# Kernel optimization log

Measured on AMD Instinct MI355X. Metric: run time of the kernel, lower is better.

The kernel has to match this reference:

```python
import jax, jax.numpy as jnp
import numpy as np

NUM_ATOMS = 65536
NUM_BONDS = 131072          # directed bonds; row NUM_BONDS is the zero sentinel h(-1)
MAX_NBR = 4
ATOM_FDIM = 133
CONCAT_FDIM = 147           # atom_fdim + bond_fdim
D_HIDDEN = 300
DEPTH = 3
GF_DIM = 2048
N_MOLS = 4096               # uniform molecules: 16 atoms each


def setup_inputs() -> dict:
    key = jax.random.key(0)
    ks = jax.random.split(key, 9)
    atom_features = jax.random.normal(ks[0], (NUM_ATOMS, ATOM_FDIM), dtype=jnp.float32)
    f_ini_atoms_bonds = jax.random.normal(ks[1], (NUM_BONDS + 1, CONCAT_FDIM), dtype=jnp.float32)
    f_ini_atoms_bonds = f_ini_atoms_bonds.at[-1].set(0.0)  # h(-1) sentinel row
    # indices in [-1, NUM_BONDS-1]; -1 means 'no incoming bond' -> sentinel
    mapping = jax.random.randint(ks[2], (NUM_BONDS + 1, MAX_NBR), -1, NUM_BONDS)
    mapping = mapping.at[-1].set(-1)
    atom_to_incoming_bonds = jax.random.randint(ks[3], (NUM_ATOMS, MAX_NBR), -1, NUM_BONDS)
    global_features = jax.random.normal(ks[4], (N_MOLS, GF_DIM), dtype=jnp.float32)
    W_i = jax.random.normal(ks[5], (D_HIDDEN, CONCAT_FDIM), dtype=jnp.float32) / np.sqrt(CONCAT_FDIM)
    W_h = jax.random.normal(ks[6], (D_HIDDEN, D_HIDDEN), dtype=jnp.float32) / np.sqrt(D_HIDDEN)
    W_o = jax.random.normal(ks[7], (D_HIDDEN, ATOM_FDIM + D_HIDDEN), dtype=jnp.float32) / np.sqrt(ATOM_FDIM + D_HIDDEN)
    b_o = jax.random.normal(ks[8], (D_HIDDEN,), dtype=jnp.float32) * 0.01
    return {
        'atom_features': atom_features,
        'f_ini_atoms_bonds': f_ini_atoms_bonds,
        'atom_to_incoming_bonds': atom_to_incoming_bonds,
        'mapping': mapping,
        'global_features': global_features,
        'W_i': W_i, 'W_h': W_h, 'W_o': W_o, 'b_o': b_o,
    }


def reference(atom_features, f_ini_atoms_bonds, atom_to_incoming_bonds, mapping,
              global_features, W_i, W_h, W_o, b_o):
    nb1 = f_ini_atoms_bonds.shape[0]          # num_bonds + 1 (last row = zero sentinel)
    sentinel = nb1 - 1
    # -1 padding indexes the zero sentinel row (torch negative-index trick)
    map_idx = jnp.where(mapping < 0, sentinel, mapping)
    a2b_idx = jnp.where(atom_to_incoming_bonds < 0, sentinel, atom_to_incoming_bonds)

    inp = f_ini_atoms_bonds @ W_i.T           # [nb1, d_hidden]
    h_message = jax.nn.relu(inp)
    for _ in range(1, DEPTH):                 # depth-1 message passing steps
        message = h_message[map_idx].sum(axis=1)          # gather-sum over incoming bonds
        h_message = jax.nn.relu(inp + message @ W_h.T)    # (dropout p=0 omitted)

    # atom readout: sum incoming bond hidden states per atom
    messages = h_message[a2b_idx].sum(axis=1)             # [num_atoms, d_hidden]
    atoms_hidden = jax.nn.relu(
        jnp.concatenate([atom_features, messages], axis=1) @ W_o.T + b_o)

    # mean readout per molecule (uniform molecule size)
    n_mols = global_features.shape[0]
    d = atoms_hidden.shape[-1]
    mol_vecs = atoms_hidden.reshape(n_mols, -1, d).mean(axis=1)
    return jnp.concatenate([mol_vecs, global_features], axis=1)
```

## Files before the change

kernel.cpp:

```cpp
#include <hip/hip_runtime.h>

typedef short bf16x8 __attribute__((ext_vector_type(8)));
typedef float f32x4 __attribute__((ext_vector_type(4)));

constexpr int NB1    = 131073;
constexpr int SENT   = 131072;
constexpr int NATOMS = 65536;
constexpr int AFD    = 133;
constexpr int CFD    = 147;
constexpr int DH     = 300;
constexpr int GFD    = 2048;
constexpr int NMOLS  = 4096;
constexpr int OUTD   = DH + GFD;
constexpr int HS     = 320;
constexpr int KP1    = 160;
constexpr int KP2    = 320;
constexpr int KPC    = 480;
constexpr int LSTR   = 328;
constexpr int LSTRC  = 488;

__device__ __forceinline__ unsigned short f2b(float f) {
    unsigned u = __float_as_uint(f);
    u += 0x7fffu + ((u >> 16) & 1u);
    return (unsigned short)(u >> 16);
}
__device__ __forceinline__ float blo(unsigned x) { return __uint_as_float(x << 16); }
__device__ __forceinline__ float bhi(unsigned x) { return __uint_as_float(x & 0xffff0000u); }
__device__ __forceinline__ unsigned pk2(float hi, float lo) {
    return ((unsigned)f2b(hi) << 16) | (unsigned)f2b(lo);
}
__device__ __forceinline__ unsigned pairsum4(unsigned a, unsigned b, unsigned c, unsigned d) {
    float lo = blo(a) + blo(b) + blo(c) + blo(d);
    float hi = bhi(a) + bhi(b) + bhi(c) + bhi(d);
    return pk2(hi, lo);
}
__device__ __forceinline__ bf16x8 asbf(uint4 u) {
    union { uint4 u; bf16x8 b; } c; c.u = u; return c.b;
}


__global__ __launch_bounds__(256, 2) void fused_in(
    const float* __restrict__ fini,
    const unsigned short* __restrict__ WiP,
    const unsigned short* __restrict__ WhP,
    unsigned short* __restrict__ inp,
    unsigned short* __restrict__ y1)
{
    __shared__ __align__(16) short As[64 * LSTR];
    const int tid = threadIdx.x, w = tid >> 6, lane = tid & 63;
    const int ml = lane & 15, kl = lane >> 4;
    const int m0 = blockIdx.x * 64;

    f32x4 acc[4][5];
#pragma unroll
    for (int mt = 0; mt < 4; ++mt)
#pragma unroll
        for (int nt = 0; nt < 5; ++nt) acc[mt][nt] = (f32x4){0.f, 0.f, 0.f, 0.f};

    const float* fr[4];
#pragma unroll
    for (int mt = 0; mt < 4; ++mt) {
        int r = m0 + mt * 16 + ml;
        fr[mt] = fini + (size_t)(r < NB1 ? r : SENT) * CFD + kl * 8;
    }
    const unsigned short* bpi = WiP + (size_t)(w * 80 + ml) * KP1 + kl * 8;
#pragma unroll
    for (int c = 0; c < 5; ++c) {
        uint4 B[5];
#pragma unroll
        for (int nt = 0; nt < 5; ++nt) B[nt] = *(const uint4*)(bpi + c * 32 + nt * 16 * KP1);
        bf16x8 af[4];
#pragma unroll
        for (int mt = 0; mt < 4; ++mt) {
            union { short s[8]; bf16x8 x; } u;
            if (c < 4) {
#pragma unroll
                for (int j = 0; j < 8; ++j) u.s[j] = (short)f2b(fr[mt][c * 32 + j]);
            } else {
#pragma unroll
                for (int j = 0; j < 8; ++j) {
                    int k = 128 + kl * 8 + j;
                    u.s[j] = (short)f2b(k < CFD ? fr[mt][c * 32 + j] : 0.f);
                }
            }
            af[mt] = u.x;
        }
#pragma unroll
        for (int mt = 0; mt < 4; ++mt)
#pragma unroll
            for (int nt = 0; nt < 5; ++nt)
                acc[mt][nt] = __builtin_amdgcn_mfma_f32_16x16x32_bf16(af[mt], asbf(B[nt]), acc[mt][nt], 0, 0, 0);
    }

#pragma unroll
    for (int mt = 0; mt < 4; ++mt)
#pragma unroll
        for (int reg = 0; reg < 4; ++reg) {
            int lr = mt * 16 + kl * 4 + reg;
            int m = m0 + lr;
#pragma unroll
            for (int nt = 0; nt < 5; ++nt) {
                int col = w * 80 + nt * 16 + ml;
                float v = acc[mt][nt][reg];
                if (m < NB1) inp[(size_t)m * HS + col] = f2b(v);
                As[lr * LSTR + col] = (short)f2b(v > 0.f ? v : 0.f);
            }
        }
    __syncthreads();

#pragma unroll
    for (int mt = 0; mt < 4; ++mt)
#pragma unroll
        for (int nt = 0; nt < 5; ++nt) acc[mt][nt] = (f32x4){0.f, 0.f, 0.f, 0.f};
    const unsigned short* bph = WhP + (size_t)(w * 80 + ml) * KP2 + kl * 8;
#pragma unroll
    for (int c = 0; c < 10; ++c) {
        uint4 B[5];
#pragma unroll
        for (int nt = 0; nt < 5; ++nt) B[nt] = *(const uint4*)(bph + c * 32 + nt * 16 * KP2);
        bf16x8 af[4];
#pragma unroll
        for (int mt = 0; mt < 4; ++mt)
            af[mt] = *(const bf16x8*)&As[(mt * 16 + ml) * LSTR + c * 32 + kl * 8];
#pragma unroll
        for (int mt = 0; mt < 4; ++mt)
#pragma unroll
            for (int nt = 0; nt < 5; ++nt)
                acc[mt][nt] = __builtin_amdgcn_mfma_f32_16x16x32_bf16(af[mt], asbf(B[nt]), acc[mt][nt], 0, 0, 0);
    }
#pragma unroll
    for (int mt = 0; mt < 4; ++mt)
#pragma unroll
        for (int reg = 0; reg < 4; ++reg) {
            int m = m0 + mt * 16 + kl * 4 + reg;
            if (m < NB1) {
#pragma unroll
                for (int nt = 0; nt < 5; ++nt)
                    y1[(size_t)m * HS + w * 80 + nt * 16 + ml] = f2b(acc[mt][nt][reg]);
            }
        }
}

__global__ __launch_bounds__(256, 2) void fused_mid(
    const unsigned short* __restrict__ ysrc,
    const unsigned short* __restrict__ inp,
    const int* __restrict__ mapping,
    const unsigned short* __restrict__ WhP,
    unsigned short* __restrict__ ydst)
{
    __shared__ __align__(16) short As[64 * LSTR];
    const int tid = threadIdx.x, w = tid >> 6, lane = tid & 63;
    const int ml = lane & 15, kl = lane >> 4;
    const int m0 = blockIdx.x * 64;

    {
        const int sr = tid & 63, sg = tid >> 6;
        int srow = m0 + sr;
        int crow = srow < NB1 ? srow : SENT;
        int4 mp = *(const int4*)(mapping + (size_t)crow * 4);
        const unsigned short* r0 = ysrc + (size_t)(mp.x < 0 ? SENT : mp.x) * HS;
        const unsigned short* r1 = ysrc + (size_t)(mp.y < 0 ? SENT : mp.y) * HS;
        const unsigned short* r2 = ysrc + (size_t)(mp.z < 0 ? SENT : mp.z) * HS;
        const unsigned short* r3 = ysrc + (size_t)(mp.w < 0 ? SENT : mp.w) * HS;
        const unsigned short* ip = inp + (size_t)crow * HS;
#pragma unroll
        for (int s = 0; s < 10; ++s) {
            int off = (s * 4 + sg) * 8;
            uint4 a = *(const uint4*)(r0 + off);
            uint4 b = *(const uint4*)(r1 + off);
            uint4 c = *(const uint4*)(r2 + off);
            uint4 d = *(const uint4*)(r3 + off);
            uint4 e = *(const uint4*)(ip + off);
            uint4 o;
            float lo, hi;
            lo = blo(a.x)+blo(b.x)+blo(c.x)+blo(d.x)+blo(e.x); hi = bhi(a.x)+bhi(b.x)+bhi(c.x)+bhi(d.x)+bhi(e.x);
            o.x = pk2(hi > 0.f ? hi : 0.f, lo > 0.f ? lo : 0.f);
            lo = blo(a.y)+blo(b.y)+blo(c.y)+blo(d.y)+blo(e.y); hi = bhi(a.y)+bhi(b.y)+bhi(c.y)+bhi(d.y)+bhi(e.y);
            o.y = pk2(hi > 0.f ? hi : 0.f, lo > 0.f ? lo : 0.f);
            lo = blo(a.z)+blo(b.z)+blo(c.z)+blo(d.z)+blo(e.z); hi = bhi(a.z)+bhi(b.z)+bhi(c.z)+bhi(d.z)+bhi(e.z);
            o.z = pk2(hi > 0.f ? hi : 0.f, lo > 0.f ? lo : 0.f);
            lo = blo(a.w)+blo(b.w)+blo(c.w)+blo(d.w)+blo(e.w); hi = bhi(a.w)+bhi(b.w)+bhi(c.w)+bhi(d.w)+bhi(e.w);
            o.w = pk2(hi > 0.f ? hi : 0.f, lo > 0.f ? lo : 0.f);
            *(uint4*)&As[sr * LSTR + off] = o;
        }
    }
    __syncthreads();

    f32x4 acc[4][5];
#pragma unroll
    for (int mt = 0; mt < 4; ++mt)
#pragma unroll
        for (int nt = 0; nt < 5; ++nt) acc[mt][nt] = (f32x4){0.f, 0.f, 0.f, 0.f};
    const unsigned short* bph = WhP + (size_t)(w * 80 + ml) * KP2 + kl * 8;
#pragma unroll
    for (int c = 0; c < 10; ++c) {
        uint4 B[5];
#pragma unroll
        for (int nt = 0; nt < 5; ++nt) B[nt] = *(const uint4*)(bph + c * 32 + nt * 16 * KP2);
        bf16x8 af[4];
#pragma unroll
        for (int mt = 0; mt < 4; ++mt)
            af[mt] = *(const bf16x8*)&As[(mt * 16 + ml) * LSTR + c * 32 + kl * 8];
#pragma unroll
        for (int mt = 0; mt < 4; ++mt)
#pragma unroll
            for (int nt = 0; nt < 5; ++nt)
                acc[mt][nt] = __builtin_amdgcn_mfma_f32_16x16x32_bf16(af[mt], asbf(B[nt]), acc[mt][nt], 0, 0, 0);
    }
#pragma unroll
    for (int mt = 0; mt < 4; ++mt)
#pragma unroll
        for (int reg = 0; reg < 4; ++reg) {
            int m = m0 + mt * 16 + kl * 4 + reg;
            if (m < NB1) {
#pragma unroll
                for (int nt = 0; nt < 5; ++nt)
                    ydst[(size_t)m * HS + w * 80 + nt * 16 + ml] = f2b(acc[mt][nt][reg]);
            }
        }
}

__global__ __launch_bounds__(256) void gather_bond(
    const unsigned short* __restrict__ y, const unsigned short* __restrict__ inp,
    const int* __restrict__ mapping, unsigned short* __restrict__ hout)
{
    int t = blockIdx.x * 256 + threadIdx.x;
    int row = t >> 3, g = t & 7;
    if (row >= NB1) return;
    int4 mp = *(const int4*)(mapping + (size_t)row * 4);
    const unsigned short* r0 = y + (size_t)(mp.x < 0 ? SENT : mp.x) * HS;
    const unsigned short* r1 = y + (size_t)(mp.y < 0 ? SENT : mp.y) * HS;
    const unsigned short* r2 = y + (size_t)(mp.z < 0 ? SENT : mp.z) * HS;
    const unsigned short* r3 = y + (size_t)(mp.w < 0 ? SENT : mp.w) * HS;
    const unsigned short* ip = inp + (size_t)row * HS;
    unsigned short* op = hout + (size_t)row * HS;
#pragma unroll
    for (int s = 0; s < 5; ++s) {
        int off = (g + s * 8) * 8;
        uint4 a = *(const uint4*)(r0 + off);
        uint4 b = *(const uint4*)(r1 + off);
        uint4 c = *(const uint4*)(r2 + off);
        uint4 d = *(const uint4*)(r3 + off);
        uint4 e = *(const uint4*)(ip + off);
        uint4 o;
        float lo, hi;
        lo = blo(a.x)+blo(b.x)+blo(c.x)+blo(d.x)+blo(e.x); hi = bhi(a.x)+bhi(b.x)+bhi(c.x)+bhi(d.x)+bhi(e.x);
        o.x = pk2(hi > 0.f ? hi : 0.f, lo > 0.f ? lo : 0.f);
        lo = blo(a.y)+blo(b.y)+blo(c.y)+blo(d.y)+blo(e.y); hi = bhi(a.y)+bhi(b.y)+bhi(c.y)+bhi(d.y)+bhi(e.y);
        o.y = pk2(hi > 0.f ? hi : 0.f, lo > 0.f ? lo : 0.f);
        lo = blo(a.z)+blo(b.z)+blo(c.z)+blo(d.z)+blo(e.z); hi = bhi(a.z)+bhi(b.z)+bhi(c.z)+bhi(d.z)+bhi(e.z);
        o.z = pk2(hi > 0.f ? hi : 0.f, lo > 0.f ? lo : 0.f);
        lo = blo(a.w)+blo(b.w)+blo(c.w)+blo(d.w)+blo(e.w); hi = bhi(a.w)+bhi(b.w)+bhi(c.w)+bhi(d.w)+bhi(e.w);
        o.w = pk2(hi > 0.f ? hi : 0.f, lo > 0.f ? lo : 0.f);
        *(uint4*)(op + off) = o;
    }
}

__global__ __launch_bounds__(256, 2) void fused_atom(
    const float* __restrict__ atomf,
    const unsigned short* __restrict__ h,
    const int* __restrict__ a2b,
    const unsigned short* __restrict__ WoC,
    const float* __restrict__ bo,
    float* __restrict__ out)
{
    __shared__ __align__(16) short As[64 * LSTRC];
    const int tid = threadIdx.x, w = tid >> 6, lane = tid & 63;
    const int ml = lane & 15, kl = lane >> 4;
    const int m0 = blockIdx.x * 64;

    {
        const int sr = tid & 63, sg = tid >> 6;
        int row = m0 + sr;
        int4 mp = *(const int4*)(a2b + (size_t)row * 4);
        const unsigned short* r0 = h + (size_t)(mp.x < 0 ? SENT : mp.x) * HS;
        const unsigned short* r1 = h + (size_t)(mp.y < 0 ? SENT : mp.y) * HS;
        const unsigned short* r2 = h + (size_t)(mp.z < 0 ? SENT : mp.z) * HS;
        const unsigned short* r3 = h + (size_t)(mp.w < 0 ? SENT : mp.w) * HS;
        const float* fp = atomf + (size_t)row * AFD;
#pragma unroll
        for (int s = 0; s < 15; ++s) {
            int k0 = (s * 4 + sg) * 8;
            if (k0 < KP1) {
                union { short s8[8]; uint4 u; } u;
#pragma unroll
                for (int j = 0; j < 8; ++j) {
                    int k = k0 + j;
                    u.s8[j] = (short)f2b(k < AFD ? fp[k] : 0.f);
                }
                *(uint4*)&As[sr * LSTRC + k0] = u.u;
            } else {
                int off = k0 - KP1;
                uint4 a = *(const uint4*)(r0 + off);
                uint4 b = *(const uint4*)(r1 + off);
                uint4 c = *(const uint4*)(r2 + off);
                uint4 d = *(const uint4*)(r3 + off);
                uint4 o;
                o.x = pairsum4(a.x, b.x, c.x, d.x);
                o.y = pairsum4(a.y, b.y, c.y, d.y);
                o.z = pairsum4(a.z, b.z, c.z, d.z);
                o.w = pairsum4(a.w, b.w, c.w, d.w);
                *(uint4*)&As[sr * LSTRC + k0] = o;
            }
        }
    }
    __syncthreads();

    f32x4 acc[4][5];
#pragma unroll
    for (int mt = 0; mt < 4; ++mt)
#pragma unroll
        for (int nt = 0; nt < 5; ++nt) acc[mt][nt] = (f32x4){0.f, 0.f, 0.f, 0.f};
    const unsigned short* bp = WoC + (size_t)(w * 80 + ml) * KPC + kl * 8;
#pragma unroll
    for (int c = 0; c < 15; ++c) {
        uint4 B[5];
#pragma unroll
        for (int nt = 0; nt < 5; ++nt) B[nt] = *(const uint4*)(bp + c * 32 + nt * 16 * KPC);
        bf16x8 af[4];
#pragma unroll
        for (int mt = 0; mt < 4; ++mt)
            af[mt] = *(const bf16x8*)&As[(mt * 16 + ml) * LSTRC + c * 32 + kl * 8];
#pragma unroll
        for (int mt = 0; mt < 4; ++mt)
#pragma unroll
            for (int nt = 0; nt < 5; ++nt)
                acc[mt][nt] = __builtin_amdgcn_mfma_f32_16x16x32_bf16(af[mt], asbf(B[nt]), acc[mt][nt], 0, 0, 0);
    }

#pragma unroll
    for (int mt = 0; mt < 4; ++mt) {
        int mol = blockIdx.x * 4 + mt;
#pragma unroll
        for (int nt = 0; nt < 5; ++nt) {
            int n = w * 80 + nt * 16 + ml;
            float bias = (n < DH) ? bo[n] : 0.f;
            float s = 0.f;
#pragma unroll
            for (int reg = 0; reg < 4; ++reg) {
                float v = acc[mt][nt][reg] + bias;
                s += (v > 0.f ? v : 0.f);
            }
            s += __shfl_down(s, 32, 64);
            s += __shfl_down(s, 16, 64);
            if (kl == 0 && n < DH) out[(size_t)mol * OUTD + n] = s * (1.f / 16.f);
        }
    }
}


__global__ __launch_bounds__(256, 3) void bond_gemm_fb(
    const float* __restrict__ fini, const unsigned short* __restrict__ hsrc,
    const int* __restrict__ mapping, const unsigned short* __restrict__ WiP,
    const unsigned short* __restrict__ WhP, unsigned short* __restrict__ hdst,
    int do_msg)
{
    const int tid = threadIdx.x, wv = tid >> 6, lane = tid & 63;
    const int ml = lane & 15, kh = lane >> 4;
    const int m0 = blockIdx.x * 64 + wv * 16;
    const int mrow = m0 + ml;
    const int mrowc = mrow < NB1 ? mrow : SENT;

    f32x4 acc[20];
#pragma unroll
    for (int nt = 0; nt < 20; ++nt) acc[nt] = (f32x4){0.f, 0.f, 0.f, 0.f};
    {
        const float* fp = fini + (size_t)mrowc * CFD;
#pragma unroll
        for (int c = 0; c < 5; ++c) {
            union { short s[8]; bf16x8 x; } u;
#pragma unroll
            for (int j = 0; j < 8; ++j) {
                int k = c * 32 + kh * 8 + j;
                u.s[j] = (short)f2b(k < CFD ? fp[k] : 0.f);
            }
            const unsigned short* bp = WiP + ml * KP1 + c * 32 + kh * 8;
#pragma unroll
            for (int nt = 0; nt < 20; ++nt)
                acc[nt] = __builtin_amdgcn_mfma_f32_16x16x32_bf16(u.x, *(const bf16x8*)(bp + nt * 16 * KP1), acc[nt], 0, 0, 0);
        }
    }
    if (do_msg) {
        int4 mp = *(const int4*)(mapping + (size_t)mrowc * 4);
        const unsigned short* g0 = hsrc + (size_t)(mp.x < 0 ? SENT : mp.x) * HS + kh * 8;
        const unsigned short* g1 = hsrc + (size_t)(mp.y < 0 ? SENT : mp.y) * HS + kh * 8;
        const unsigned short* g2 = hsrc + (size_t)(mp.z < 0 ? SENT : mp.z) * HS + kh * 8;
        const unsigned short* g3 = hsrc + (size_t)(mp.w < 0 ? SENT : mp.w) * HS + kh * 8;
#pragma unroll
        for (int c = 0; c < 10; ++c) {
            uint4 a = *(const uint4*)(g0 + c * 32);
            uint4 b = *(const uint4*)(g1 + c * 32);
            uint4 cc = *(const uint4*)(g2 + c * 32);
            uint4 d = *(const uint4*)(g3 + c * 32);
            uint4 o;
            o.x = pairsum4(a.x, b.x, cc.x, d.x);
            o.y = pairsum4(a.y, b.y, cc.y, d.y);
            o.z = pairsum4(a.z, b.z, cc.z, d.z);
            o.w = pairsum4(a.w, b.w, cc.w, d.w);
            const unsigned short* bp = WhP + ml * KP2 + c * 32 + kh * 8;
#pragma unroll
            for (int nt = 0; nt < 20; ++nt)
                acc[nt] = __builtin_amdgcn_mfma_f32_16x16x32_bf16(asbf(o), *(const bf16x8*)(bp + nt * 16 * KP2), acc[nt], 0, 0, 0);
        }
    }
#pragma unroll
    for (int nt = 0; nt < 20; ++nt) {
        int n = nt * 16 + ml;
#pragma unroll
        for (int reg = 0; reg < 4; ++reg) {
            int m = m0 + kh * 4 + reg;
            if (m < NB1) {
                float v = acc[nt][reg];
                hdst[(size_t)m * HS + n] = f2b(v > 0.f ? v : 0.f);
            }
        }
    }
}

__global__ __launch_bounds__(256, 3) void atom_gemm_fb(
    const float* __restrict__ atomf, const unsigned short* __restrict__ hsrc,
    const int* __restrict__ a2b, const unsigned short* __restrict__ WoA,
    const unsigned short* __restrict__ WoB, const float* __restrict__ bo,
    float* __restrict__ out)
{
    const int tid = threadIdx.x, wv = tid >> 6, lane = tid & 63;
    const int ml = lane & 15, kh = lane >> 4;
    const int m0 = blockIdx.x * 64 + wv * 16;
    const int arow = m0 + ml;

    f32x4 acc[20];
#pragma unroll
    for (int nt = 0; nt < 20; ++nt) acc[nt] = (f32x4){0.f, 0.f, 0.f, 0.f};
    {
        const float* fp = atomf + (size_t)arow * AFD;
#pragma unroll
        for (int c = 0; c < 5; ++c) {
            union { short s[8]; bf16x8 x; } u;
#pragma unroll
            for (int j = 0; j < 8; ++j) {
                int k = c * 32 + kh * 8 + j;
                u.s[j] = (short)f2b(k < AFD ? fp[k] : 0.f);
            }
            const unsigned short* bp = WoA + ml * KP1 + c * 32 + kh * 8;
#pragma unroll
            for (int nt = 0; nt < 20; ++nt)
                acc[nt] = __builtin_amdgcn_mfma_f32_16x16x32_bf16(u.x, *(const bf16x8*)(bp + nt * 16 * KP1), acc[nt], 0, 0, 0);
        }
    }
    {
        int4 mp = *(const int4*)(a2b + (size_t)arow * 4);
        const unsigned short* g0 = hsrc + (size_t)(mp.x < 0 ? SENT : mp.x) * HS + kh * 8;
        const unsigned short* g1 = hsrc + (size_t)(mp.y < 0 ? SENT : mp.y) * HS + kh * 8;
        const unsigned short* g2 = hsrc + (size_t)(mp.z < 0 ? SENT : mp.z) * HS + kh * 8;
        const unsigned short* g3 = hsrc + (size_t)(mp.w < 0 ? SENT : mp.w) * HS + kh * 8;
#pragma unroll
        for (int c = 0; c < 10; ++c) {
            uint4 a = *(const uint4*)(g0 + c * 32);
            uint4 b = *(const uint4*)(g1 + c * 32);
            uint4 cc = *(const uint4*)(g2 + c * 32);
            uint4 d = *(const uint4*)(g3 + c * 32);
            uint4 o;
            o.x = pairsum4(a.x, b.x, cc.x, d.x);
            o.y = pairsum4(a.y, b.y, cc.y, d.y);
            o.z = pairsum4(a.z, b.z, cc.z, d.z);
            o.w = pairsum4(a.w, b.w, cc.w, d.w);
            const unsigned short* bp = WoB + ml * KP2 + c * 32 + kh * 8;
#pragma unroll
            for (int nt = 0; nt < 20; ++nt)
                acc[nt] = __builtin_amdgcn_mfma_f32_16x16x32_bf16(asbf(o), *(const bf16x8*)(bp + nt * 16 * KP2), acc[nt], 0, 0, 0);
        }
    }
    const int mol = blockIdx.x * 4 + wv;
#pragma unroll
    for (int nt = 0; nt < 20; ++nt) {
        int n = nt * 16 + ml;
        float bias = (n < DH) ? bo[n] : 0.f;
        float s = 0.f;
#pragma unroll
        for (int reg = 0; reg < 4; ++reg) {
            float v = acc[nt][reg] + bias;
            s += (v > 0.f ? v : 0.f);
        }
        s += __shfl_down(s, 32, 64);
        s += __shfl_down(s, 16, 64);
        if (kh == 0 && n < DH) out[(size_t)mol * OUTD + n] = s * (1.f / 16.f);
    }
}


__global__ void prep_w(const float* __restrict__ Wi, const float* __restrict__ Wh,
                       const float* __restrict__ Wo, unsigned short* __restrict__ wb, int mode) {
    int t = blockIdx.x * blockDim.x + threadIdx.x;
    if (t >= 307200) return;
    float v = 0.f;
    if (t < 51200) {
        int n = t / 160, k = t % 160;
        if (n < DH && k < CFD) v = Wi[n * CFD + k];
    } else if (t < 153600) {
        int q = t - 51200; int n = q / 320, k = q % 320;
        if (n < DH && k < DH) v = Wh[n * DH + k];
    } else if (mode) {
        int q = t - 153600; int n = q / 480, k = q % 480;
        if (n < DH) {
            if (k < AFD) v = Wo[n * 433 + k];
            else if (k >= 160 && k < 460) v = Wo[n * 433 + AFD + (k - 160)];
        }
    } else if (t < 204800) {
        int q = t - 153600; int n = q / 160, k = q % 160;
        if (n < DH && k < AFD) v = Wo[n * 433 + k];
    } else {
        int q = t - 204800; int n = q / 320, k = q % 320;
        if (n < DH && k < DH) v = Wo[n * 433 + AFD + k];
    }
    wb[t] = f2b(v);
}

__global__ void copy_gf(const float4* __restrict__ gf, float* __restrict__ out) {
    int t = blockIdx.x * blockDim.x + threadIdx.x;
    if (t >= NMOLS * (GFD / 4)) return;
    int mol = t >> 9;
    int g4 = t & 511;
    float4 v = gf[t];
    *(float4*)(out + (size_t)mol * OUTD + DH + g4 * 4) = v;
}

extern "C" void kernel_launch(void* const* d_in, const int* in_sizes, int n_in,
                              void* d_out, int out_size, void* d_ws, size_t ws_size,
                              hipStream_t stream) {
    const float* atomf   = (const float*)d_in[0];
    const float* fini    = (const float*)d_in[1];
    const int*   a2b     = (const int*)d_in[2];
    const int*   mapping = (const int*)d_in[3];
    const float* gf      = (const float*)d_in[4];
    const float* W_i     = (const float*)d_in[5];
    const float* W_h     = (const float*)d_in[6];
    const float* W_o     = (const float*)d_in[7];
    const float* b_o     = (const float*)d_in[8];
    float* out = (float*)d_out;

    char* ws = (char*)d_ws;
    size_t SA = (((size_t)NB1 * HS * 2) + 255) & ~(size_t)255;
    size_t SW = 307200 * 2;
    dim3 blk(256);

    if (ws_size >= 3 * SA + SW) {
        unsigned short* inp = (unsigned short*)ws;
        unsigned short* y1  = (unsigned short*)(ws + SA);
        unsigned short* y2  = (unsigned short*)(ws + 2 * SA);
        unsigned short* wb  = (unsigned short*)(ws + 3 * SA);
        unsigned short* WiP = wb;
        unsigned short* WhP = wb + 51200;
        unsigned short* WoC = wb + 153600;
        unsigned short* h2  = y1;

        prep_w<<<1200, blk, 0, stream>>>(W_i, W_h, W_o, wb, 1);
        fused_in<<<2049, blk, 0, stream>>>(fini, WiP, WhP, inp, y1);
        fused_mid<<<2049, blk, 0, stream>>>(y1, inp, mapping, WhP, y2);
        gather_bond<<<4097, blk, 0, stream>>>(y2, inp, mapping, h2);
        fused_atom<<<1024, blk, 0, stream>>>(atomf, h2, a2b, WoC, b_o, out);
    } else {
        unsigned short* h_a = (unsigned short*)ws;
        unsigned short* h_b = (unsigned short*)(ws + SA);
        unsigned short* wb  = (unsigned short*)(ws + 2 * SA);
        unsigned short* WiP = wb;
        unsigned short* WhP = wb + 51200;
        unsigned short* WoA = wb + 153600;
        unsigned short* WoB = wb + 204800;

        prep_w<<<1200, blk, 0, stream>>>(W_i, W_h, W_o, wb, 0);
        bond_gemm_fb<<<2049, blk, 0, stream>>>(fini, h_a, mapping, WiP, WhP, h_a, 0);
        bond_gemm_fb<<<2049, blk, 0, stream>>>(fini, h_a, mapping, WiP, WhP, h_b, 1);
        bond_gemm_fb<<<2049, blk, 0, stream>>>(fini, h_b, mapping, WiP, WhP, h_a, 1);
        atom_gemm_fb<<<1024, blk, 0, stream>>>(atomf, h_a, a2b, WoA, WoB, b_o, out);
    }
    copy_gf<<<NMOLS * (GFD / 4) / 256, blk, 0, stream>>>((const float4*)gf, out);
}
```

Baseline: 584.3 us.

## Stage GEMM inputs/outputs through LDS and pre-swizzle weights into MFMA fragment order

Loads the fp32 bond and atom feature rows cooperatively into shared memory with contiguous per-thread accesses, instead of strided per-lane fragment reads in the MFMA loop. Epilogues now write accumulators to LDS first and then store full 16-byte rows to global memory, which keeps the writes coalesced. The weight prep kernel lays the weights out in per-lane MFMA fragment order, so each B load is one contiguous 16-byte access per lane. This adds extra barriers and LDS round-trips in exchange for better global memory coalescing.

New measurement: 554.2 us. 1.05x faster.

```diff
diff --git a/kernel.cpp b/kernel.cpp
--- a/kernel.cpp
+++ b/kernel.cpp
@@ -34,6 +34,15 @@
     float hi = bhi(a) + bhi(b) + bhi(c) + bhi(d);
     return pk2(hi, lo);
 }
+__device__ __forceinline__ unsigned relu_pk(unsigned u) {
+    unsigned lo = (u & 0x8000u) ? 0u : (u & 0xFFFFu);
+    unsigned hi = (u & 0x80000000u) ? 0u : (u & 0xFFFF0000u);
+    return lo | hi;
+}
+__device__ __forceinline__ uint4 relu4(uint4 v) {
+    v.x = relu_pk(v.x); v.y = relu_pk(v.y); v.z = relu_pk(v.z); v.w = relu_pk(v.w);
+    return v;
+}
 __device__ __forceinline__ bf16x8 asbf(uint4 u) {
     union { uint4 u; bf16x8 b; } c; c.u = u; return c.b;
 }
@@ -41,8 +50,8 @@
 
 __global__ __launch_bounds__(256, 2) void fused_in(
     const float* __restrict__ fini,
-    const unsigned short* __restrict__ WiP,
-    const unsigned short* __restrict__ WhP,
+    const unsigned short* __restrict__ WiF,
+    const unsigned short* __restrict__ WhF,
     unsigned short* __restrict__ inp,
     unsigned short* __restrict__ y1)
 {
@@ -51,73 +60,75 @@
     const int ml = lane & 15, kl = lane >> 4;
     const int m0 = blockIdx.x * 64;
 
+#pragma unroll
+    for (int i = 0; i < 20; ++i) {
+        int f = tid + i * 256;
+        int row = f / 80, p = f - row * 80;
+        int k = p * 2;
+        int m = m0 + row;
+        const float* src = fini + (size_t)(m < NB1 ? m : SENT) * CFD;
+        float v0 = (k < CFD) ? src[k] : 0.f;
+        float v1 = (k + 1 < CFD) ? src[k + 1] : 0.f;
+        *(unsigned*)&As[row * LSTR + k] = ((unsigned)f2b(v1) << 16) | (unsigned)f2b(v0);
+    }
+    __syncthreads();
+
     f32x4 acc[4][5];
 #pragma unroll
     for (int mt = 0; mt < 4; ++mt)
 #pragma unroll
         for (int nt = 0; nt < 5; ++nt) acc[mt][nt] = (f32x4){0.f, 0.f, 0.f, 0.f};
 
-    const float* fr[4];
-#pragma unroll
-    for (int mt = 0; mt < 4; ++mt) {
-        int r = m0 + mt * 16 + ml;
-        fr[mt] = fini + (size_t)(r < NB1 ? r : SENT) * CFD + kl * 8;
-    }
-    const unsigned short* bpi = WiP + (size_t)(w * 80 + ml) * KP1 + kl * 8;
 #pragma unroll
     for (int c = 0; c < 5; ++c) {
         uint4 B[5];
 #pragma unroll
-        for (int nt = 0; nt < 5; ++nt) B[nt] = *(const uint4*)(bpi + c * 32 + nt * 16 * KP1);
+        for (int nt = 0; nt < 5; ++nt)
+            B[nt] = *(const uint4*)(WiF + (size_t)((c * 20 + w * 5 + nt) * 64 + lane) * 8);
         bf16x8 af[4];
 #pragma unroll
-        for (int mt = 0; mt < 4; ++mt) {
-            union { short s[8]; bf16x8 x; } u;
-            if (c < 4) {
-#pragma unroll
-                for (int j = 0; j < 8; ++j) u.s[j] = (short)f2b(fr[mt][c * 32 + j]);
-            } else {
-#pragma unroll
-                for (int j = 0; j < 8; ++j) {
-                    int k = 128 + kl * 8 + j;
-                    u.s[j] = (short)f2b(k < CFD ? fr[mt][c * 32 + j] : 0.f);
-                }
-            }
-            af[mt] = u.x;
-        }
+        for (int mt = 0; mt < 4; ++mt)
+            af[mt] = *(const bf16x8*)&As[(mt * 16 + ml) * LSTR + c * 32 + kl * 8];
 #pragma unroll
         for (int mt = 0; mt < 4; ++mt)
 #pragma unroll
             for (int nt = 0; nt < 5; ++nt)
                 acc[mt][nt] = __builtin_amdgcn_mfma_f32_16x16x32_bf16(af[mt], asbf(B[nt]), acc[mt][nt], 0, 0, 0);
     }
+    __syncthreads();
 
 #pragma unroll
     for (int mt = 0; mt < 4; ++mt)
 #pragma unroll
         for (int reg = 0; reg < 4; ++reg) {
             int lr = mt * 16 + kl * 4 + reg;
-            int m = m0 + lr;
-#pragma unroll
-            for (int nt = 0; nt < 5; ++nt) {
-                int col = w * 80 + nt * 16 + ml;
-                float v = acc[mt][nt][reg];
-                if (m < NB1) inp[(size_t)m * HS + col] = f2b(v);
-                As[lr * LSTR + col] = (short)f2b(v > 0.f ? v : 0.f);
-            }
-        }
+#pragma unroll
+            for (int nt = 0; nt < 5; ++nt)
+                As[lr * LSTR + w * 80 + nt * 16 + ml] = (short)f2b(acc[mt][nt][reg]);
+        }
+    __syncthreads();
+
+#pragma unroll
+    for (int i = 0; i < 10; ++i) {
+        int f = tid + i * 256;
+        int row = f / 40, s = f - row * 40;
+        uint4 v = *(const uint4*)&As[row * LSTR + s * 8];
+        int m = m0 + row;
+        if (m < NB1) *(uint4*)(inp + (size_t)m * HS + s * 8) = v;
+        *(uint4*)&As[row * LSTR + s * 8] = relu4(v);
+    }
     __syncthreads();
 
 #pragma unroll
     for (int mt = 0; mt < 4; ++mt)
 #pragma unroll
         for (int nt = 0; nt < 5; ++nt) acc[mt][nt] = (f32x4){0.f, 0.f, 0.f, 0.f};
-    const unsigned short* bph = WhP + (size_t)(w * 80 + ml) * KP2 + kl * 8;
 #pragma unroll
     for (int c = 0; c < 10; ++c) {
         uint4 B[5];
 #pragma unroll
-        for (int nt = 0; nt < 5; ++nt) B[nt] = *(const uint4*)(bph + c * 32 + nt * 16 * KP2);
+        for (int nt = 0; nt < 5; ++nt)
+            B[nt] = *(const uint4*)(WhF + (size_t)((c * 20 + w * 5 + nt) * 64 + lane) * 8);
         bf16x8 af[4];
 #pragma unroll
         for (int mt = 0; mt < 4; ++mt)
@@ -128,24 +139,32 @@
             for (int nt = 0; nt < 5; ++nt)
                 acc[mt][nt] = __builtin_amdgcn_mfma_f32_16x16x32_bf16(af[mt], asbf(B[nt]), acc[mt][nt], 0, 0, 0);
     }
+    __syncthreads();
 #pragma unroll
     for (int mt = 0; mt < 4; ++mt)
 #pragma unroll
         for (int reg = 0; reg < 4; ++reg) {
-            int m = m0 + mt * 16 + kl * 4 + reg;
-            if (m < NB1) {
-#pragma unroll
-                for (int nt = 0; nt < 5; ++nt)
-                    y1[(size_t)m * HS + w * 80 + nt * 16 + ml] = f2b(acc[mt][nt][reg]);
-            }
-        }
+            int lr = mt * 16 + kl * 4 + reg;
+#pragma unroll
+            for (int nt = 0; nt < 5; ++nt)
+                As[lr * LSTR + w * 80 + nt * 16 + ml] = (short)f2b(acc[mt][nt][reg]);
+        }
+    __syncthreads();
+#pragma unroll
+    for (int i = 0; i < 10; ++i) {
+        int f = tid + i * 256;
+        int row = f / 40, s = f - row * 40;
+        int m = m0 + row;
+        if (m < NB1)
+            *(uint4*)(y1 + (size_t)m * HS + s * 8) = *(const uint4*)&As[row * LSTR + s * 8];
+    }
 }
 
 __global__ __launch_bounds__(256, 2) void fused_mid(
     const unsigned short* __restrict__ ysrc,
     const unsigned short* __restrict__ inp,
     const int* __restrict__ mapping,
-    const unsigned short* __restrict__ WhP,
+    const unsigned short* __restrict__ WhF,
     unsigned short* __restrict__ ydst)
 {
     __shared__ __align__(16) short As[64 * LSTR];
@@ -191,12 +210,12 @@
     for (int mt = 0; mt < 4; ++mt)
 #pragma unroll
         for (int nt = 0; nt < 5; ++nt) acc[mt][nt] = (f32x4){0.f, 0.f, 0.f, 0.f};
-    const unsigned short* bph = WhP + (size_t)(w * 80 + ml) * KP2 + kl * 8;
 #pragma unroll
     for (int c = 0; c < 10; ++c) {
         uint4 B[5];
 #pragma unroll
-        for (int nt = 0; nt < 5; ++nt) B[nt] = *(const uint4*)(bph + c * 32 + nt * 16 * KP2);
+        for (int nt = 0; nt < 5; ++nt)
+            B[nt] = *(const uint4*)(WhF + (size_t)((c * 20 + w * 5 + nt) * 64 + lane) * 8);
         bf16x8 af[4];
 #pragma unroll
         for (int mt = 0; mt < 4; ++mt)
@@ -207,17 +226,25 @@
             for (int nt = 0; nt < 5; ++nt)
                 acc[mt][nt] = __builtin_amdgcn_mfma_f32_16x16x32_bf16(af[mt], asbf(B[nt]), acc[mt][nt], 0, 0, 0);
     }
+    __syncthreads();
 #pragma unroll
     for (int mt = 0; mt < 4; ++mt)
 #pragma unroll
         for (int reg = 0; reg < 4; ++reg) {
-            int m = m0 + mt * 16 + kl * 4 + reg;
-            if (m < NB1) {
-#pragma unroll
-                for (int nt = 0; nt < 5; ++nt)
-                    ydst[(size_t)m * HS + w * 80 + nt * 16 + ml] = f2b(acc[mt][nt][reg]);
-            }
-        }
+            int lr = mt * 16 + kl * 4 + reg;
+#pragma unroll
+            for (int nt = 0; nt < 5; ++nt)
+                As[lr * LSTR + w * 80 + nt * 16 + ml] = (short)f2b(acc[mt][nt][reg]);
+        }
+    __syncthreads();
+#pragma unroll
+    for (int i = 0; i < 10; ++i) {
+        int f = tid + i * 256;
+        int row = f / 40, s = f - row * 40;
+        int m = m0 + row;
+        if (m < NB1)
+            *(uint4*)(ydst + (size_t)m * HS + s * 8) = *(const uint4*)&As[row * LSTR + s * 8];
+    }
 }
 
 __global__ __launch_bounds__(256) void gather_bond(
@@ -260,7 +287,7 @@
     const float* __restrict__ atomf,
     const unsigned short* __restrict__ h,
     const int* __restrict__ a2b,
-    const unsigned short* __restrict__ WoC,
+    const unsigned short* __restrict__ WoF,
     const float* __restrict__ bo,
     float* __restrict__ out)
 {
@@ -269,6 +296,16 @@
     const int ml = lane & 15, kl = lane >> 4;
     const int m0 = blockIdx.x * 64;
 
+#pragma unroll
+    for (int i = 0; i < 20; ++i) {
+        int f = tid + i * 256;
+        int row = f / 80, p = f - row * 80;
+        int k = p * 2;
+        const float* src = atomf + (size_t)(m0 + row) * AFD;
+        float v0 = (k < AFD) ? src[k] : 0.f;
+        float v1 = (k + 1 < AFD) ? src[k + 1] : 0.f;
+        *(unsigned*)&As[row * LSTRC + k] = ((unsigned)f2b(v1) << 16) | (unsigned)f2b(v0);
+    }
     {
         const int sr = tid & 63, sg = tid >> 6;
         int row = m0 + sr;
@@ -277,31 +314,19 @@
         const unsigned short* r1 = h + (size_t)(mp.y < 0 ? SENT : mp.y) * HS;
         const unsigned short* r2 = h + (size_t)(mp.z < 0 ? SENT : mp.z) * HS;
         const unsigned short* r3 = h + (size_t)(mp.w < 0 ? SENT : mp.w) * HS;
-        const float* fp = atomf + (size_t)row * AFD;
-#pragma unroll
-        for (int s = 0; s < 15; ++s) {
-            int k0 = (s * 4 + sg) * 8;
-            if (k0 < KP1) {
-                union { short s8[8]; uint4 u; } u;
-#pragma unroll
-                for (int j = 0; j < 8; ++j) {
-                    int k = k0 + j;
-                    u.s8[j] = (short)f2b(k < AFD ? fp[k] : 0.f);
-                }
-                *(uint4*)&As[sr * LSTRC + k0] = u.u;
-            } else {
-                int off = k0 - KP1;
-                uint4 a = *(const uint4*)(r0 + off);
-                uint4 b = *(const uint4*)(r1 + off);
-                uint4 c = *(const uint4*)(r2 + off);
-                uint4 d = *(const uint4*)(r3 + off);
-                uint4 o;
-                o.x = pairsum4(a.x, b.x, c.x, d.x);
-                o.y = pairsum4(a.y, b.y, c.y, d.y);
-                o.z = pairsum4(a.z, b.z, c.z, d.z);
-                o.w = pairsum4(a.w, b.w, c.w, d.w);
-                *(uint4*)&As[sr * LSTRC + k0] = o;
-            }
+#pragma unroll
+        for (int s = 0; s < 10; ++s) {
+            int off = (s * 4 + sg) * 8;
+            uint4 a = *(const uint4*)(r0 + off);
+            uint4 b = *(const uint4*)(r1 + off);
+            uint4 c = *(const uint4*)(r2 + off);
+            uint4 d = *(const uint4*)(r3 + off);
+            uint4 o;
+            o.x = pairsum4(a.x, b.x, c.x, d.x);
+            o.y = pairsum4(a.y, b.y, c.y, d.y);
+            o.z = pairsum4(a.z, b.z, c.z, d.z);
+            o.w = pairsum4(a.w, b.w, c.w, d.w);
+            *(uint4*)&As[sr * LSTRC + KP1 + off] = o;
         }
     }
     __syncthreads();
@@ -311,12 +336,12 @@
     for (int mt = 0; mt < 4; ++mt)
 #pragma unroll
         for (int nt = 0; nt < 5; ++nt) acc[mt][nt] = (f32x4){0.f, 0.f, 0.f, 0.f};
-    const unsigned short* bp = WoC + (size_t)(w * 80 + ml) * KPC + kl * 8;
 #pragma unroll
     for (int c = 0; c < 15; ++c) {
         uint4 B[5];
 #pragma unroll
-        for (int nt = 0; nt < 5; ++nt) B[nt] = *(const uint4*)(bp + c * 32 + nt * 16 * KPC);
+        for (int nt = 0; nt < 5; ++nt)
+            B[nt] = *(const uint4*)(WoF + (size_t)((c * 20 + w * 5 + nt) * 64 + lane) * 8);
         bf16x8 af[4];
 #pragma unroll
         for (int mt = 0; mt < 4; ++mt)
@@ -493,24 +518,40 @@
     int t = blockIdx.x * blockDim.x + threadIdx.x;
     if (t >= 307200) return;
     float v = 0.f;
-    if (t < 51200) {
-        int n = t / 160, k = t % 160;
-        if (n < DH && k < CFD) v = Wi[n * CFD + k];
-    } else if (t < 153600) {
-        int q = t - 51200; int n = q / 320, k = q % 320;
-        if (n < DH && k < DH) v = Wh[n * DH + k];
-    } else if (mode) {
-        int q = t - 153600; int n = q / 480, k = q % 480;
+    if (mode) {
+        int q, nchunk_base;
+        const float* W; int ld, ksz, kofs = 0;
+        if (t < 51200)       { q = t;          W = Wi; ld = CFD; ksz = CFD; }
+        else if (t < 153600) { q = t - 51200;  W = Wh; ld = DH;  ksz = DH;  }
+        else                 { q = t - 153600; W = Wo; ld = 433; ksz = 433; kofs = 1; }
+        int j = q & 7, l = (q >> 3) & 63, r = q >> 9;
+        int tile = r % 20, c = r / 20;
+        int ml = l & 15, kl = l >> 4;
+        int n = tile * 16 + ml;
+        int k = c * 32 + kl * 8 + j;
         if (n < DH) {
-            if (k < AFD) v = Wo[n * 433 + k];
-            else if (k >= 160 && k < 460) v = Wo[n * 433 + AFD + (k - 160)];
-        }
-    } else if (t < 204800) {
-        int q = t - 153600; int n = q / 160, k = q % 160;
-        if (n < DH && k < AFD) v = Wo[n * 433 + k];
+            if (!kofs) {
+                if (k < ksz) v = W[n * ld + k];
+            } else {
+                if (k < AFD) v = W[n * ld + k];
+                else if (k >= KP1 && k < KP1 + DH) v = W[n * ld + AFD + (k - KP1)];
+            }
+        }
+        (void)nchunk_base;
     } else {
-        int q = t - 204800; int n = q / 320, k = q % 320;
-        if (n < DH && k < DH) v = Wo[n * 433 + AFD + k];
+        if (t < 51200) {
+            int n = t / 160, k = t % 160;
+            if (n < DH && k < CFD) v = Wi[n * CFD + k];
+        } else if (t < 153600) {
+            int q = t - 51200; int n = q / 320, k = q % 320;
+            if (n < DH && k < DH) v = Wh[n * DH + k];
+        } else if (t < 204800) {
+            int q = t - 153600; int n = q / 160, k = q % 160;
+            if (n < DH && k < AFD) v = Wo[n * 433 + k];
+        } else {
+            int q = t - 204800; int n = q / 320, k = q % 320;
+            if (n < DH && k < DH) v = Wo[n * 433 + AFD + k];
+        }
     }
     wb[t] = f2b(v);
 }
@@ -548,16 +589,16 @@
         unsigned short* y1  = (unsigned short*)(ws + SA);
         unsigned short* y2  = (unsigned short*)(ws + 2 * SA);
         unsigned short* wb  = (unsigned short*)(ws + 3 * SA);
-        unsigned short* WiP = wb;
-        unsigned short* WhP = wb + 51200;
-        unsigned short* WoC = wb + 153600;
+        unsigned short* WiF = wb;
+        unsigned short* WhF = wb + 51200;
+        unsigned short* WoF = wb + 153600;
         unsigned short* h2  = y1;
 
         prep_w<<<1200, blk, 0, stream>>>(W_i, W_h, W_o, wb, 1);
-        fused_in<<<2049, blk, 0, stream>>>(fini, WiP, WhP, inp, y1);
-        fused_mid<<<2049, blk, 0, stream>>>(y1, inp, mapping, WhP, y2);
+        fused_in<<<2049, blk, 0, stream>>>(fini, WiF, WhF, inp, y1);
+        fused_mid<<<2049, blk, 0, stream>>>(y1, inp, mapping, WhF, y2);
         gather_bond<<<4097, blk, 0, stream>>>(y2, inp, mapping, h2);
-        fused_atom<<<1024, blk, 0, stream>>>(atomf, h2, a2b, WoC, b_o, out);
+        fused_atom<<<1024, blk, 0, stream>>>(atomf, h2, a2b, WoF, b_o, out);
     } else {
         unsigned short* h_a = (unsigned short*)ws;
         unsigned short* h_b = (unsigned short*)(ws + SA);
```
